# Performance work log

Measured on AMD Instinct MI355X. Metric: run time of the kernel, lower is better.

The kernel has to match this reference:

```python
import jax, jax.numpy as jnp
import numpy as np

B, D, H, W = 2, 256, 64, 64
NH = 4
EPS = 1e-5


def _ln(x, g, b):
    # LayerNorm over channel dim of NCHW tensor (matches permute->LN(C)->permute)
    mu = jnp.mean(x, axis=1, keepdims=True)
    var = jnp.mean((x - mu) ** 2, axis=1, keepdims=True)
    xn = (x - mu) * jax.lax.rsqrt(var + EPS)
    return xn * g[None, :, None, None] + b[None, :, None, None]


def _conv1x1(x, w, b):
    # w: (out_c, in_c)
    return jnp.einsum('bchw,oc->bohw', x, w) + b[None, :, None, None]


def _dwconv3x3(x, w, b):
    # depthwise 3x3, w: (C, 1, 3, 3)
    y = jax.lax.conv_general_dilated(
        x, w, window_strides=(1, 1), padding='SAME',
        dimension_numbers=('NCHW', 'OIHW', 'NCHW'), feature_group_count=D)
    return y + b[None, :, None, None]


def setup_inputs() -> dict:
    key = jax.random.key(0)
    ks = jax.random.split(key, 12)
    sc = 0.02

    def n(k, shape):
        return jax.random.normal(k, shape, dtype=jnp.float32) * sc

    return {
        'image_embedding': jax.random.normal(ks[0], (B, D, H, W), dtype=jnp.float32),
        'guide': jax.random.normal(ks[1], (B, D, H, W), dtype=jnp.float32),
        'ln1_g': jnp.ones((D,), jnp.float32), 'ln1_b': jnp.zeros((D,), jnp.float32),
        'ln2_g': jnp.ones((D,), jnp.float32), 'ln2_b': jnp.zeros((D,), jnp.float32),
        'qw1': n(ks[2], (D, D)), 'qb1': jnp.zeros((D,), jnp.float32),
        'qw2': n(ks[3], (D, 1, 3, 3)), 'qb2': jnp.zeros((D,), jnp.float32),
        'kw1': n(ks[4], (D, D)), 'kb1': jnp.zeros((D,), jnp.float32),
        'kw2': n(ks[5], (D, 1, 3, 3)), 'kb2': jnp.zeros((D,), jnp.float32),
        'vw1': n(ks[6], (D, D)), 'vb1': jnp.zeros((D,), jnp.float32),
        'vw2': n(ks[7], (D, 1, 3, 3)), 'vb2': jnp.zeros((D,), jnp.float32),
        'ow': n(ks[8], (D, D)), 'ob': jnp.zeros((D,), jnp.float32),
    }


def reference(image_embedding, guide, ln1_g, ln1_b, ln2_g, ln2_b,
              qw1, qb1, qw2, qb2, kw1, kb1, kw2, kb2,
              vw1, vb1, vw2, vb2, ow, ob):
    residual = image_embedding
    x = _ln(image_embedding, ln1_g, ln1_b)
    g = _ln(guide, ln2_g, ln2_b)

    q = _dwconv3x3(_conv1x1(x, qw1, qb1), qw2, qb2)
    k = _dwconv3x3(_conv1x1(g, kw1, kb1), kw2, kb2)
    v = _dwconv3x3(_conv1x1(g, vw1, vb1), vw2, vb2)

    hd = D // NH
    scale = hd ** -0.5

    def to_heads(t):  # (B,C,H,W) -> (B, NH, HW, hd)
        return t.reshape(B, NH, hd, H * W).transpose(0, 1, 3, 2)

    q = to_heads(q) * scale
    k = to_heads(k)
    v = to_heads(v)

    attn = jax.nn.softmax(jnp.einsum('bhnd,bhmd->bhnm', q, k), axis=-1)
    out = jnp.einsum('bhnm,bhmd->bhnd', attn, v)
    out = out.transpose(0, 1, 3, 2).reshape(B, D, H, W)
    out = _conv1x1(out, ow, ob)
    return residual + out
```

## Files before the change

kernel.cpp:

```cpp
#include <hip/hip_runtime.h>
#include <cstdint>
#include <cstddef>

typedef unsigned short u16;
typedef unsigned int u32;
typedef __attribute__((ext_vector_type(8))) short short8;
typedef __attribute__((ext_vector_type(4))) float f32x4;
typedef __attribute__((ext_vector_type(16))) float f32x16;
typedef __attribute__((ext_vector_type(2))) unsigned int u32x2;

#define CD 256
#define HWD 4096
#define NHD 4
#define HDD 64
#define NSPLIT 4

static __device__ __forceinline__ u16 f2b(float f) {
    u32 u = __builtin_bit_cast(u32, f);
    return (u16)((u + 0x7fffu + ((u >> 16) & 1u)) >> 16);
}
static __device__ __forceinline__ float b2f(u16 h) {
    return __builtin_bit_cast(float, (u32)h << 16);
}
static __device__ __forceinline__ u32 pk2(float a, float b) {
    return (u32)f2b(a) | ((u32)f2b(b) << 16);
}
static __device__ __forceinline__ float fexp2(float x) {
#if __has_builtin(__builtin_amdgcn_exp2f)
    return __builtin_amdgcn_exp2f(x);
#else
    return __expf(x * 0.69314718056f);
#endif
}
static __device__ __forceinline__ u32 cvtpk(float lo, float hi) {
    u32 r;
    asm("v_cvt_pk_bf16_f32 %0, %1, %2" : "=v"(r) : "v"(lo), "v"(hi));
    return r;
}
static __device__ __forceinline__ u32x2 plswap(u32 a, u32 b) {
    return __builtin_amdgcn_permlane32_swap(a, b, false, false);
}
static __device__ __forceinline__ void async16(const void* g, void* l) {
    __builtin_amdgcn_global_load_lds(
        (const __attribute__((address_space(1))) unsigned int*)g,
        (__attribute__((address_space(3))) unsigned int*)l,
        16, 0, 0);
}

__global__ __launch_bounds__(256) void ln_transpose(
    const float* __restrict__ x0, const float* __restrict__ x1,
    const float* __restrict__ g0, const float* __restrict__ b0,
    const float* __restrict__ g1, const float* __restrict__ b1,
    const float* __restrict__ qw1, const float* __restrict__ kw1,
    const float* __restrict__ vw1, const float* __restrict__ ow,
    u16* __restrict__ out0, u16* __restrict__ out1, u16* __restrict__ wbf)
{
    int bid = blockIdx.x;
    int tid = threadIdx.x;

    if (bid >= 512) {
        int base = (bid - 512) * 8192 + tid * 32;
        int which = base >> 16;
        int off = base & 65535;
        const float* s = (which == 0) ? qw1 : (which == 1) ? kw1
                       : (which == 2) ? vw1 : ow;
        s += off;
        u16* d = wbf + (size_t)which * 65536 + off;
        #pragma unroll
        for (int j = 0; j < 4; ++j) {
            float4 a = ((const float4*)s)[2 * j];
            float4 b = ((const float4*)s)[2 * j + 1];
            uint4 o;
            o.x = pk2(a.x, a.y); o.y = pk2(a.z, a.w);
            o.z = pk2(b.x, b.y); o.w = pk2(b.z, b.w);
            ((uint4*)d)[j] = o;
        }
        return;
    }

    int t = bid >> 8, b = (bid >> 7) & 1, p0 = (bid & 127) << 5;
    const float* x = t ? x1 : x0;
    const float* g = t ? g1 : g0;
    const float* bb = t ? b1 : b0;
    u16* out = t ? out1 : out0;

    int tx = tid & 31, ty = tid >> 5;
    const float* xb = x + (size_t)b * CD * HWD + p0 + tx;

    __shared__ float red[2][8][32];
    __shared__ u16 T[256][33];

    float xv[32];
    float s = 0.f, sq = 0.f;
    #pragma unroll
    for (int i = 0; i < 32; ++i) {
        float v = xb[(size_t)(ty * 32 + i) * HWD];
        xv[i] = v;
        s += v; sq += v * v;
    }
    red[0][ty][tx] = s; red[1][ty][tx] = sq;
    __syncthreads();
    float st = 0.f, sqt = 0.f;
    #pragma unroll
    for (int j = 0; j < 8; ++j) { st += red[0][j][tx]; sqt += red[1][j][tx]; }
    float mean = st * (1.f / 256.f);
    float var = sqt * (1.f / 256.f) - mean * mean;
    float rstd = rsqrtf(var + 1e-5f);

    #pragma unroll
    for (int i = 0; i < 32; ++i) {
        int c = ty * 32 + i;
        float v = (xv[i] - mean) * rstd * g[c] + bb[c];
        T[c][tx] = f2b(v);
    }
    __syncthreads();

    #pragma unroll
    for (int pass = 0; pass < 4; ++pass) {
        int idx = pass * 256 + tid;
        int p = idx >> 5, cs = (idx & 31) * 8;
        u16 tmp[8];
        #pragma unroll
        for (int j = 0; j < 8; ++j) tmp[j] = T[cs + j][p];
        *(uint4*)&out[((size_t)b * HWD + p0 + p) * CD + cs] = *(const uint4*)tmp;
    }
}

__global__ __launch_bounds__(256) void qkv_gemm(
    const u16* __restrict__ xT, const u16* __restrict__ gT,
    const u16* __restrict__ Wbf,
    const float* __restrict__ qb1, const float* __restrict__ kb1,
    const float* __restrict__ vb1,
    u16* __restrict__ q1, u16* __restrict__ k1, u16* __restrict__ v1)
{
    int z = blockIdx.z;
    int mm = z >> 1, b = z & 1;
    const u16* X    = (mm == 0) ? xT : gT;
    const u16* W    = Wbf + (size_t)mm * 65536;
    const float* Bi = (mm == 0) ? qb1 : (mm == 1) ? kb1 : vb1;
    u16* Y          = (mm == 0) ? q1 : (mm == 1) ? k1 : v1;

    int n0 = blockIdx.x * 128;
    int p0 = blockIdx.y * 64;

    __shared__ u16 As[64][72];
    __shared__ u16 Bs[128][72];

    int tid = threadIdx.x;
    int lane = tid & 63, w = tid >> 6;
    int wm = w >> 1, wn = w & 1;
    int l15 = lane & 15, quad = lane >> 4;

    f32x4 acc[2][4];
    #pragma unroll
    for (int mi = 0; mi < 2; ++mi)
        #pragma unroll
        for (int nj = 0; nj < 4; ++nj)
            acc[mi][nj] = (f32x4){0.f, 0.f, 0.f, 0.f};

    const u16* Xb = X + (size_t)b * HWD * CD;

    int arow = tid >> 2, aseg = (tid & 3) * 16;
    const u16* agp = Xb + (size_t)(p0 + arow) * CD + aseg;
    int brow = tid >> 1, bkh = (tid & 1) * 32;
    const u16* wgp = W + (size_t)(n0 + brow) * CD + bkh;

    uint4 ra0 = ((const uint4*)agp)[0], ra1 = ((const uint4*)agp)[1];
    uint4 rb0 = ((const uint4*)wgp)[0], rb1 = ((const uint4*)wgp)[1];
    uint4 rb2 = ((const uint4*)wgp)[2], rb3 = ((const uint4*)wgp)[3];

    for (int kt = 0; kt < 4; ++kt) {
        __syncthreads();
        *(uint4*)&As[arow][aseg] = ra0;
        *(uint4*)&As[arow][aseg + 8] = ra1;
        *(uint4*)&Bs[brow][bkh] = rb0;
        *(uint4*)&Bs[brow][bkh + 8] = rb1;
        *(uint4*)&Bs[brow][bkh + 16] = rb2;
        *(uint4*)&Bs[brow][bkh + 24] = rb3;
        if (kt < 3) {
            const u16* ag2 = agp + (kt + 1) * 64;
            ra0 = ((const uint4*)ag2)[0]; ra1 = ((const uint4*)ag2)[1];
            const u16* wg2 = wgp + (kt + 1) * 64;
            rb0 = ((const uint4*)wg2)[0]; rb1 = ((const uint4*)wg2)[1];
            rb2 = ((const uint4*)wg2)[2]; rb3 = ((const uint4*)wg2)[3];
        }
        __syncthreads();

        #pragma unroll
        for (int kk = 0; kk < 2; ++kk) {
            short8 af[2], bf[4];
            #pragma unroll
            for (int mi = 0; mi < 2; ++mi)
                af[mi] = *(const short8*)&As[wm * 32 + mi * 16 + l15][kk * 32 + quad * 8];
            #pragma unroll
            for (int nj = 0; nj < 4; ++nj)
                bf[nj] = *(const short8*)&Bs[wn * 64 + nj * 16 + l15][kk * 32 + quad * 8];
            #pragma unroll
            for (int mi = 0; mi < 2; ++mi)
                #pragma unroll
                for (int nj = 0; nj < 4; ++nj)
                    acc[mi][nj] = __builtin_amdgcn_mfma_f32_16x16x32_bf16(
                        af[mi], bf[nj], acc[mi][nj], 0, 0, 0);
        }
    }

    u16* Yb = Y + (size_t)b * HWD * CD;
    float bias[4];
    #pragma unroll
    for (int nj = 0; nj < 4; ++nj)
        bias[nj] = Bi[n0 + wn * 64 + nj * 16 + l15];
    #pragma unroll
    for (int mi = 0; mi < 2; ++mi) {
        #pragma unroll
        for (int r = 0; r < 4; ++r) {
            int p = p0 + wm * 32 + mi * 16 + quad * 4 + r;
            #pragma unroll
            for (int nj = 0; nj < 4; ++nj) {
                int ch = n0 + wn * 64 + nj * 16 + l15;
                Yb[(size_t)p * CD + ch] = f2b(acc[mi][nj][r] + bias[nj]);
            }
        }
    }
}

#define LOADROW(r, hh)                                                      \
    if ((hh) < 0 || (hh) >= 64) {                                           \
        _Pragma("unroll") for (int j = 0; j < 18; ++j) r[j] = 0.f;          \
    } else {                                                                \
        const u16* rp = inb + (size_t)((hh) * 64) * CD;                     \
        r[0] = (w0 > 0) ? b2f(rp[(size_t)(w0 - 1) * CD]) : 0.f;             \
        _Pragma("unroll") for (int j = 1; j <= 16; ++j)                     \
            r[j] = b2f(rp[(size_t)(w0 - 1 + j) * CD]);                      \
        r[17] = (w0 < 48) ? b2f(rp[(size_t)(w0 + 16) * CD]) : 0.f;          \
    }

#define CONVROW(hh, ra, rb, rc)                                             \
    {                                                                       \
        float accv[16];                                                     \
        _Pragma("unroll") for (int pi = 0; pi < 16; ++pi)                   \
            accv[pi] = bias                                                 \
              + w9[0] * ra[pi] + w9[1] * ra[pi + 1] + w9[2] * ra[pi + 2]    \
              + w9[3] * rb[pi] + w9[4] * rb[pi + 1] + w9[5] * rb[pi + 2]    \
              + w9[6] * rc[pi] + w9[7] * rc[pi + 1] + w9[8] * rc[pi + 2];   \
        int p0 = (hh) * 64 + w0;                                            \
        if (which == 2) {                                                   \
            u32 w8[8];                                                      \
            _Pragma("unroll") for (int j = 0; j < 8; ++j)                   \
                w8[j] = pk2(accv[2 * j], accv[2 * j + 1]);                  \
            uint4* dst = (uint4*)(Vt + ((size_t)(b * CD + c)) * HWD + p0);  \
            dst[0] = make_uint4(w8[0], w8[1], w8[2], w8[3]);                \
            dst[1] = make_uint4(w8[4], w8[5], w8[6], w8[7]);                \
        } else {                                                            \
            u16* outp = ((which == 0) ? Q : K) + (size_t)b * HWD * CD;      \
            _Pragma("unroll") for (int pi = 0; pi < 16; ++pi)               \
                outp[(size_t)(p0 + pi) * CD + c] = f2b(accv[pi] * oscale);  \
        }                                                                   \
    }

__global__ __launch_bounds__(256) void dwconv_nc(
    const u16* __restrict__ q1, const u16* __restrict__ k1, const u16* __restrict__ v1,
    const float* __restrict__ qw2, const float* __restrict__ qb2,
    const float* __restrict__ kw2, const float* __restrict__ kb2,
    const float* __restrict__ vw2, const float* __restrict__ vb2,
    u16* __restrict__ Q, u16* __restrict__ K, u16* __restrict__ Vt)
{
    int bid = blockIdx.x;
    int which = bid >> 8;
    int rem = bid & 255;
    int b = rem >> 7;
    int hp = (rem >> 2) & 31;
    int ws = rem & 3;
    int h0 = hp * 2, w0 = ws * 16;

    const u16* in = ((which == 0) ? q1 : (which == 1) ? k1 : v1) + (size_t)b * HWD * CD;
    const float* wsrc = (which == 0) ? qw2 : (which == 1) ? kw2 : vw2;
    const float* bsrc = (which == 0) ? qb2 : (which == 1) ? kb2 : vb2;
    float oscale = (which == 0) ? 0.18033688011112042f : 1.0f;

    int c = threadIdx.x;
    float w9[9];
    #pragma unroll
    for (int j = 0; j < 9; ++j) w9[j] = wsrc[c * 9 + j];
    float bias = bsrc[c];

    const u16* inb = in + c;

    float r0[18], r1[18], r2[18];
    LOADROW(r0, h0 - 1)
    LOADROW(r1, h0)
    LOADROW(r2, h0 + 1)
    CONVROW(h0, r0, r1, r2)
    LOADROW(r0, h0 + 2)
    CONVROW(h0 + 1, r1, r2, r0)
}

__global__ __launch_bounds__(256, 4) void attn_kernel(
    const u16* __restrict__ Q, const u16* __restrict__ K,
    const u16* __restrict__ Vt, u16* __restrict__ Opart,
    float* __restrict__ Psum)
{
    int qt = blockIdx.x;
    int bh = blockIdx.y;
    int ks = blockIdx.z;
    int b = bh >> 2, nh = bh & 3;

    __shared__ u16 Ks_[2][64 * 64];
    __shared__ u16 Vs_[2][64 * 64];

    int tid = threadIdx.x;
    int lane = tid & 63, w = tid >> 6;
    int l31 = lane & 31, h = lane >> 5;
    int sw = l31 & 7;

    const u16* Qb = Q + ((size_t)b * HWD) * CD + nh * 64;
    const u16* Kb = K + ((size_t)b * HWD) * CD + nh * 64;
    const u16* Vb = Vt + ((size_t)bh * HDD) * HWD;

    int q0 = qt * 128 + w * 32;

    short8 qf[4];
    #pragma unroll
    for (int si = 0; si < 4; ++si)
        qf[si] = *(const short8*)(Qb + (size_t)(q0 + l31) * CD + si * 16 + h * 8);

    int rr = lane >> 3;
    int gseg = (lane & 7) ^ rr;
    const u16* kgb = Kb + (size_t)(ks * 1024 + w * 16 + rr) * CD + gseg * 8;
    const u16* vgb = Vb + (size_t)(w * 16 + rr) * HWD + ks * 1024 + gseg * 8;

    f32x16 acc[2];
    #pragma unroll
    for (int db = 0; db < 2; ++db)
        #pragma unroll
        for (int r = 0; r < 16; ++r) acc[db][r] = 0.f;
    float psum = 0.f;

    #pragma unroll
    for (int j = 0; j < 2; ++j) {
        async16(kgb + (size_t)(j * 8) * CD, &Ks_[0][(w * 16 + j * 8) * 64]);
        async16(vgb + (size_t)(j * 8) * HWD, &Vs_[0][(w * 16 + j * 8) * 64]);
    }

    for (int it = 0; it < 16; ++it) {
        int cur = it & 1;
        __syncthreads();
        if (it + 1 < 16) {
            int nxt = cur ^ 1;
            #pragma unroll
            for (int j = 0; j < 2; ++j) {
                async16(kgb + (size_t)((it + 1) * 64 + j * 8) * CD,
                        &Ks_[nxt][(w * 16 + j * 8) * 64]);
                async16(vgb + (size_t)(j * 8) * HWD + (it + 1) * 64,
                        &Vs_[nxt][(w * 16 + j * 8) * 64]);
            }
        }

        #pragma unroll
        for (int kb = 0; kb < 2; ++kb) {
            short8 kf[4];
            #pragma unroll
            for (int si = 0; si < 4; ++si)
                kf[si] = *(const short8*)&Ks_[cur][(kb * 32 + l31) * 64 +
                                                   (((si * 2 + h) ^ sw) << 3)];
            f32x16 st;
            #pragma unroll
            for (int r = 0; r < 16; ++r) st[r] = 0.f;
            __builtin_amdgcn_s_setprio(1);
            #pragma unroll
            for (int si = 0; si < 4; ++si)
                st = __builtin_amdgcn_mfma_f32_32x32x16_bf16(
                    kf[si], qf[si], st, 0, 0, 0);
            __builtin_amdgcn_s_setprio(0);

            float e[16];
            #pragma unroll
            for (int r = 0; r < 16; ++r) e[r] = fexp2(st[r]);
            #pragma unroll
            for (int r = 0; r < 16; r += 4)
                psum += (e[r] + e[r + 1]) + (e[r + 2] + e[r + 3]);

            u32 wv[8];
            #pragma unroll
            for (int m = 0; m < 8; ++m) wv[m] = cvtpk(e[2 * m], e[2 * m + 1]);
            u32x2 s02 = plswap(wv[0], wv[2]);
            u32x2 s13 = plswap(wv[1], wv[3]);
            u32x2 s46 = plswap(wv[4], wv[6]);
            u32x2 s57 = plswap(wv[5], wv[7]);
            union { u32 u[4]; short8 s8; } p0_, p1_;
            p0_.u[0] = s02.x; p0_.u[1] = s13.x; p0_.u[2] = s02.y; p0_.u[3] = s13.y;
            p1_.u[0] = s46.x; p1_.u[1] = s57.x; p1_.u[2] = s46.y; p1_.u[3] = s57.y;

            #pragma unroll
            for (int db = 0; db < 2; ++db) {
                short8 vf0 = *(const short8*)&Vs_[cur][(db * 32 + l31) * 64 +
                                 ((((kb * 2 + 0) * 2 + h) ^ sw) << 3)];
                short8 vf1 = *(const short8*)&Vs_[cur][(db * 32 + l31) * 64 +
                                 ((((kb * 2 + 1) * 2 + h) ^ sw) << 3)];
                __builtin_amdgcn_s_setprio(1);
                acc[db] = __builtin_amdgcn_mfma_f32_32x32x16_bf16(
                    p0_.s8, vf0, acc[db], 0, 0, 0);
                acc[db] = __builtin_amdgcn_mfma_f32_32x32x16_bf16(
                    p1_.s8, vf1, acc[db], 0, 0, 0);
                __builtin_amdgcn_s_setprio(0);
            }
        }
    }

    u16* Ob = Opart + (((size_t)ks * 8 + bh) * HWD) * HDD;
    #pragma unroll
    for (int db = 0; db < 2; ++db)
        #pragma unroll
        for (int r = 0; r < 16; ++r) {
            int n = q0 + (r & 3) + 8 * (r >> 2) + 4 * h;
            Ob[(size_t)n * HDD + db * 32 + l31] = f2b(acc[db][r]);
        }

    float s = psum + __shfl_xor(psum, 32);
    float* Pb = Psum + ((size_t)ks * 8 + bh) * HWD + q0;
    if (lane < 32) Pb[lane] = s;
}

__global__ __launch_bounds__(256) void out_gemm(
    const u16* __restrict__ Wo, const float* __restrict__ Bi,
    const u16* __restrict__ Opart, const float* __restrict__ Psum,
    const float* __restrict__ residual, float* __restrict__ out)
{
    int b = blockIdx.z;
    int m0 = blockIdx.y * 64;
    int n0 = blockIdx.x * 64;

    __shared__ u16 As[64][40];
    __shared__ u16 Bs[64][40];

    int tid = threadIdx.x;
    int lane = tid & 63, w = tid >> 6;
    int wm = w >> 1, wn = w & 1;
    int l15 = lane & 15, quad = lane >> 4;

    f32x4 acc[2][2];
    #pragma unroll
    for (int mi = 0; mi < 2; ++mi)
        #pragma unroll
        for (int nj = 0; nj < 2; ++nj)
            acc[mi][nj] = (f32x4){0.f, 0.f, 0.f, 0.f};

    int arow = tid >> 2, aseg = (tid & 3) * 8;
    const u16* wgp = Wo + (size_t)(m0 + arow) * CD + aseg;
    int brow = tid >> 2, bseg = (tid & 3) * 8;
    int pn = n0 + brow;

    uint4 ra = *(const uint4*)wgp;

    uint4 ro[NSPLIT]; float rinv;
    {
        int c = bseg;
        int bh = b * 4 + (c >> 6), d0 = c & 63;
        float p = 0.f;
        #pragma unroll
        for (int s = 0; s < NSPLIT; ++s) {
            ro[s] = *(const uint4*)&Opart[(((size_t)s * 8 + bh) * HWD + pn) * HDD + d0];
            p += Psum[((size_t)s * 8 + bh) * HWD + pn];
        }
        rinv = 1.f / p;
    }

    for (int kt = 0; kt < 8; ++kt) {
        __syncthreads();
        *(uint4*)&As[arow][aseg] = ra;
        {
            float v[8];
            #pragma unroll
            for (int j = 0; j < 8; ++j) v[j] = 0.f;
            #pragma unroll
            for (int s = 0; s < NSPLIT; ++s) {
                u16 t[8];
                *(uint4*)t = ro[s];
                #pragma unroll
                for (int j = 0; j < 8; ++j) v[j] += b2f(t[j]);
            }
            uint4 bb;
            bb.x = pk2(v[0] * rinv, v[1] * rinv);
            bb.y = pk2(v[2] * rinv, v[3] * rinv);
            bb.z = pk2(v[4] * rinv, v[5] * rinv);
            bb.w = pk2(v[6] * rinv, v[7] * rinv);
            *(uint4*)&Bs[brow][bseg] = bb;
        }
        if (kt < 7) {
            ra = *(const uint4*)(wgp + (kt + 1) * 32);
            int c = (kt + 1) * 32 + bseg;
            int bh = b * 4 + (c >> 6), d0 = c & 63;
            float p = 0.f;
            #pragma unroll
            for (int s = 0; s < NSPLIT; ++s) {
                ro[s] = *(const uint4*)&Opart[(((size_t)s * 8 + bh) * HWD + pn) * HDD + d0];
                p += Psum[((size_t)s * 8 + bh) * HWD + pn];
            }
            rinv = 1.f / p;
        }
        __syncthreads();

        short8 af[2], bf[2];
        #pragma unroll
        for (int mi = 0; mi < 2; ++mi)
            af[mi] = *(const short8*)&As[wm * 32 + mi * 16 + l15][quad * 8];
        #pragma unroll
        for (int nj = 0; nj < 2; ++nj)
            bf[nj] = *(const short8*)&Bs[wn * 32 + nj * 16 + l15][quad * 8];
        #pragma unroll
        for (int mi = 0; mi < 2; ++mi)
            #pragma unroll
            for (int nj = 0; nj < 2; ++nj)
                acc[mi][nj] = __builtin_amdgcn_mfma_f32_16x16x32_bf16(
                    af[mi], bf[nj], acc[mi][nj], 0, 0, 0);
    }

    #pragma unroll
    for (int mi = 0; mi < 2; ++mi) {
        int mb = m0 + wm * 32 + mi * 16 + quad * 4;
        #pragma unroll
        for (int r = 0; r < 4; ++r) {
            float bias = Bi[mb + r];
            const float* res = residual + (size_t)(b * CD + mb + r) * HWD;
            float* o = out + (size_t)(b * CD + mb + r) * HWD;
            #pragma unroll
            for (int nj = 0; nj < 2; ++nj) {
                int n = n0 + wn * 32 + nj * 16 + l15;
                o[n] = acc[mi][nj][r] + bias + res[n];
            }
        }
    }
}

extern "C" void kernel_launch(void* const* d_in, const int* in_sizes, int n_in,
                              void* d_out, int out_size, void* d_ws, size_t ws_size,
                              hipStream_t stream) {
    (void)in_sizes; (void)n_in; (void)out_size; (void)ws_size;

    const float* image = (const float*)d_in[0];
    const float* guide = (const float*)d_in[1];
    const float* ln1_g = (const float*)d_in[2];
    const float* ln1_b = (const float*)d_in[3];
    const float* ln2_g = (const float*)d_in[4];
    const float* ln2_b = (const float*)d_in[5];
    const float* qw1 = (const float*)d_in[6];
    const float* qb1 = (const float*)d_in[7];
    const float* qw2 = (const float*)d_in[8];
    const float* qb2 = (const float*)d_in[9];
    const float* kw1 = (const float*)d_in[10];
    const float* kb1 = (const float*)d_in[11];
    const float* kw2 = (const float*)d_in[12];
    const float* kb2 = (const float*)d_in[13];
    const float* vw1 = (const float*)d_in[14];
    const float* vb1 = (const float*)d_in[15];
    const float* vw2 = (const float*)d_in[16];
    const float* vb2 = (const float*)d_in[17];
    const float* ow  = (const float*)d_in[18];
    const float* ob  = (const float*)d_in[19];
    float* out = (float*)d_out;

    char* ws = (char*)d_ws;
    u16* xT    = (u16*)(ws + (size_t)0  * (1 << 20));
    u16* gT    = (u16*)(ws + (size_t)4  * (1 << 20));
    u16* q1    = (u16*)(ws + (size_t)8  * (1 << 20));
    u16* k1    = (u16*)(ws + (size_t)12 * (1 << 20));
    u16* v1    = (u16*)(ws + (size_t)16 * (1 << 20));
    u16* Qh    = (u16*)(ws + (size_t)20 * (1 << 20));
    u16* Kh    = (u16*)(ws + (size_t)24 * (1 << 20));
    u16* Vt    = (u16*)(ws + (size_t)28 * (1 << 20));
    u16*   Opart = (u16*)(ws + (size_t)0  * (1 << 20));
    float* Psum  = (float*)(ws + (size_t)18 * (1 << 20));
    u16*   Wbf   = (u16*)(ws + (size_t)33 * (1 << 20));

    ln_transpose<<<dim3(544), dim3(256), 0, stream>>>(
        image, guide, ln1_g, ln1_b, ln2_g, ln2_b,
        qw1, kw1, vw1, ow, xT, gT, Wbf);

    qkv_gemm<<<dim3(2, 64, 6), dim3(256), 0, stream>>>(
        xT, gT, Wbf, qb1, kb1, vb1, q1, k1, v1);

    dwconv_nc<<<dim3(768), dim3(256), 0, stream>>>(
        q1, k1, v1, qw2, qb2, kw2, kb2, vw2, vb2, Qh, Kh, Vt);

    attn_kernel<<<dim3(32, 8, NSPLIT), dim3(256), 0, stream>>>(Qh, Kh, Vt, Opart, Psum);

    out_gemm<<<dim3(64, 4, 2), dim3(256), 0, stream>>>(
        Wbf + (size_t)3 * 65536, ob, Opart, Psum, image, out);
}
```

Before: 176.0 us.

## Load full K=256 tiles into XOR-swizzled LDS in qkv and out GEMMs

Both the QKV projection GEMM and the output GEMM now load the whole 256-deep K dimension for a 64x64 tile into shared memory at once, using an XOR swizzle on 16-byte chunks to avoid bank conflicts. This removes the per-K-step sync loop. The QKV GEMM's N tile shrinks from 128 to 64, doubling the grid to get more blocks. The cost is 64 KB of LDS per block, which may limit occupancy, plus more global loads in flight per thread and more re-reads of the activations.

New measurement: 188.3 us. +7.0%, slower.

```diff
diff --git a/kernel.cpp b/kernel.cpp
--- a/kernel.cpp
+++ b/kernel.cpp
@@ -140,83 +140,75 @@
     const float* Bi = (mm == 0) ? qb1 : (mm == 1) ? kb1 : vb1;
     u16* Y          = (mm == 0) ? q1 : (mm == 1) ? k1 : v1;
 
-    int n0 = blockIdx.x * 128;
+    int n0 = blockIdx.x * 64;
     int p0 = blockIdx.y * 64;
 
-    __shared__ u16 As[64][72];
-    __shared__ u16 Bs[128][72];
+    __shared__ u16 As[64 * 256];
+    __shared__ u16 Bs[64 * 256];
 
     int tid = threadIdx.x;
     int lane = tid & 63, w = tid >> 6;
     int wm = w >> 1, wn = w & 1;
     int l15 = lane & 15, quad = lane >> 4;
-
-    f32x4 acc[2][4];
+    int sw = l15 & 7;
+
+    int row = tid >> 2, seg = tid & 3;
+    const u16* agp = X + ((size_t)b * HWD + p0 + row) * CD + seg * 64;
+    const u16* wgp = W + (size_t)(n0 + row) * CD + seg * 64;
+
+    uint4 ra[8], rb[8];
+    #pragma unroll
+    for (int j = 0; j < 8; ++j) ra[j] = ((const uint4*)agp)[j];
+    #pragma unroll
+    for (int j = 0; j < 8; ++j) rb[j] = ((const uint4*)wgp)[j];
+
+    #pragma unroll
+    for (int j = 0; j < 8; ++j) {
+        int ch = (seg * 8 + j) ^ (row & 7);
+        *(uint4*)&As[row * 256 + ch * 8] = ra[j];
+        *(uint4*)&Bs[row * 256 + ch * 8] = rb[j];
+    }
+    __syncthreads();
+
+    f32x4 acc[2][2];
     #pragma unroll
     for (int mi = 0; mi < 2; ++mi)
         #pragma unroll
-        for (int nj = 0; nj < 4; ++nj)
+        for (int nj = 0; nj < 2; ++nj)
             acc[mi][nj] = (f32x4){0.f, 0.f, 0.f, 0.f};
 
-    const u16* Xb = X + (size_t)b * HWD * CD;
-
-    int arow = tid >> 2, aseg = (tid & 3) * 16;
-    const u16* agp = Xb + (size_t)(p0 + arow) * CD + aseg;
-    int brow = tid >> 1, bkh = (tid & 1) * 32;
-    const u16* wgp = W + (size_t)(n0 + brow) * CD + bkh;
-
-    uint4 ra0 = ((const uint4*)agp)[0], ra1 = ((const uint4*)agp)[1];
-    uint4 rb0 = ((const uint4*)wgp)[0], rb1 = ((const uint4*)wgp)[1];
-    uint4 rb2 = ((const uint4*)wgp)[2], rb3 = ((const uint4*)wgp)[3];
-
-    for (int kt = 0; kt < 4; ++kt) {
-        __syncthreads();
-        *(uint4*)&As[arow][aseg] = ra0;
-        *(uint4*)&As[arow][aseg + 8] = ra1;
-        *(uint4*)&Bs[brow][bkh] = rb0;
-        *(uint4*)&Bs[brow][bkh + 8] = rb1;
-        *(uint4*)&Bs[brow][bkh + 16] = rb2;
-        *(uint4*)&Bs[brow][bkh + 24] = rb3;
-        if (kt < 3) {
-            const u16* ag2 = agp + (kt + 1) * 64;
-            ra0 = ((const uint4*)ag2)[0]; ra1 = ((const uint4*)ag2)[1];
-            const u16* wg2 = wgp + (kt + 1) * 64;
-            rb0 = ((const uint4*)wg2)[0]; rb1 = ((const uint4*)wg2)[1];
-            rb2 = ((const uint4*)wg2)[2]; rb3 = ((const uint4*)wg2)[3];
-        }
-        __syncthreads();
-
-        #pragma unroll
-        for (int kk = 0; kk < 2; ++kk) {
-            short8 af[2], bf[4];
-            #pragma unroll
-            for (int mi = 0; mi < 2; ++mi)
-                af[mi] = *(const short8*)&As[wm * 32 + mi * 16 + l15][kk * 32 + quad * 8];
-            #pragma unroll
-            for (int nj = 0; nj < 4; ++nj)
-                bf[nj] = *(const short8*)&Bs[wn * 64 + nj * 16 + l15][kk * 32 + quad * 8];
-            #pragma unroll
-            for (int mi = 0; mi < 2; ++mi)
-                #pragma unroll
-                for (int nj = 0; nj < 4; ++nj)
-                    acc[mi][nj] = __builtin_amdgcn_mfma_f32_16x16x32_bf16(
-                        af[mi], bf[nj], acc[mi][nj], 0, 0, 0);
-        }
+    #pragma unroll
+    for (int ks = 0; ks < 8; ++ks) {
+        short8 af[2], bf[2];
+        #pragma unroll
+        for (int mi = 0; mi < 2; ++mi)
+            af[mi] = *(const short8*)&As[(wm * 32 + mi * 16 + l15) * 256 +
+                                         (((ks * 4 + quad) ^ sw) << 3)];
+        #pragma unroll
+        for (int nj = 0; nj < 2; ++nj)
+            bf[nj] = *(const short8*)&Bs[(wn * 32 + nj * 16 + l15) * 256 +
+                                         (((ks * 4 + quad) ^ sw) << 3)];
+        #pragma unroll
+        for (int mi = 0; mi < 2; ++mi)
+            #pragma unroll
+            for (int nj = 0; nj < 2; ++nj)
+                acc[mi][nj] = __builtin_amdgcn_mfma_f32_16x16x32_bf16(
+                    af[mi], bf[nj], acc[mi][nj], 0, 0, 0);
     }
 
     u16* Yb = Y + (size_t)b * HWD * CD;
-    float bias[4];
-    #pragma unroll
-    for (int nj = 0; nj < 4; ++nj)
-        bias[nj] = Bi[n0 + wn * 64 + nj * 16 + l15];
+    float bias[2];
+    #pragma unroll
+    for (int nj = 0; nj < 2; ++nj)
+        bias[nj] = Bi[n0 + wn * 32 + nj * 16 + l15];
     #pragma unroll
     for (int mi = 0; mi < 2; ++mi) {
         #pragma unroll
         for (int r = 0; r < 4; ++r) {
             int p = p0 + wm * 32 + mi * 16 + quad * 4 + r;
             #pragma unroll
-            for (int nj = 0; nj < 4; ++nj) {
-                int ch = n0 + wn * 64 + nj * 16 + l15;
+            for (int nj = 0; nj < 2; ++nj) {
+                int ch = n0 + wn * 32 + nj * 16 + l15;
                 Yb[(size_t)p * CD + ch] = f2b(acc[mi][nj][r] + bias[nj]);
             }
         }
@@ -429,13 +421,60 @@
     int m0 = blockIdx.y * 64;
     int n0 = blockIdx.x * 64;
 
-    __shared__ u16 As[64][40];
-    __shared__ u16 Bs[64][40];
+    __shared__ u16 As[64 * 256];
+    __shared__ u16 Bs[64 * 256];
 
     int tid = threadIdx.x;
     int lane = tid & 63, w = tid >> 6;
     int wm = w >> 1, wn = w & 1;
     int l15 = lane & 15, quad = lane >> 4;
+    int sw = l15 & 7;
+
+    int row = tid >> 2, seg = tid & 3;
+
+    const u16* wgp = Wo + (size_t)(m0 + row) * CD + seg * 64;
+    uint4 ra[8];
+    #pragma unroll
+    for (int j = 0; j < 8; ++j) ra[j] = ((const uint4*)wgp)[j];
+
+    int pn = n0 + row;
+    int bh = b * 4 + seg;
+    float p = 0.f;
+    #pragma unroll
+    for (int s = 0; s < NSPLIT; ++s)
+        p += Psum[((size_t)s * 8 + bh) * HWD + pn];
+    float rinv = 1.f / p;
+
+    uint4 rb[8];
+    #pragma unroll
+    for (int j = 0; j < 8; ++j) {
+        float v[8];
+        #pragma unroll
+        for (int k = 0; k < 8; ++k) v[k] = 0.f;
+        #pragma unroll
+        for (int s = 0; s < NSPLIT; ++s) {
+            uint4 t4 = *(const uint4*)&Opart[
+                (((size_t)s * 8 + bh) * HWD + pn) * HDD + j * 8];
+            u16 tt[8];
+            *(uint4*)tt = t4;
+            #pragma unroll
+            for (int k = 0; k < 8; ++k) v[k] += b2f(tt[k]);
+        }
+        uint4 o;
+        o.x = pk2(v[0] * rinv, v[1] * rinv);
+        o.y = pk2(v[2] * rinv, v[3] * rinv);
+        o.z = pk2(v[4] * rinv, v[5] * rinv);
+        o.w = pk2(v[6] * rinv, v[7] * rinv);
+        rb[j] = o;
+    }
+
+    #pragma unroll
+    for (int j = 0; j < 8; ++j) {
+        int ch = (seg * 8 + j) ^ (row & 7);
+        *(uint4*)&As[row * 256 + ch * 8] = ra[j];
+        *(uint4*)&Bs[row * 256 + ch * 8] = rb[j];
+    }
+    __syncthreads();
 
     f32x4 acc[2][2];
     #pragma unroll
@@ -444,68 +483,17 @@
         for (int nj = 0; nj < 2; ++nj)
             acc[mi][nj] = (f32x4){0.f, 0.f, 0.f, 0.f};
 
-    int arow = tid >> 2, aseg = (tid & 3) * 8;
-    const u16* wgp = Wo + (size_t)(m0 + arow) * CD + aseg;
-    int brow = tid >> 2, bseg = (tid & 3) * 8;
-    int pn = n0 + brow;
-
-    uint4 ra = *(const uint4*)wgp;
-
-    uint4 ro[NSPLIT]; float rinv;
-    {
-        int c = bseg;
-        int bh = b * 4 + (c >> 6), d0 = c & 63;
-        float p = 0.f;
-        #pragma unroll
-        for (int s = 0; s < NSPLIT; ++s) {
-            ro[s] = *(const uint4*)&Opart[(((size_t)s * 8 + bh) * HWD + pn) * HDD + d0];
-            p += Psum[((size_t)s * 8 + bh) * HWD + pn];
-        }
-        rinv = 1.f / p;
-    }
-
-    for (int kt = 0; kt < 8; ++kt) {
-        __syncthreads();
-        *(uint4*)&As[arow][aseg] = ra;
-        {
-            float v[8];
-            #pragma unroll
-            for (int j = 0; j < 8; ++j) v[j] = 0.f;
-            #pragma unroll
-            for (int s = 0; s < NSPLIT; ++s) {
-                u16 t[8];
-                *(uint4*)t = ro[s];
-                #pragma unroll
-                for (int j = 0; j < 8; ++j) v[j] += b2f(t[j]);
-            }
-            uint4 bb;
-            bb.x = pk2(v[0] * rinv, v[1] * rinv);
-            bb.y = pk2(v[2] * rinv, v[3] * rinv);
-            bb.z = pk2(v[4] * rinv, v[5] * rinv);
-            bb.w = pk2(v[6] * rinv, v[7] * rinv);
-            *(uint4*)&Bs[brow][bseg] = bb;
-        }
-        if (kt < 7) {
-            ra = *(const uint4*)(wgp + (kt + 1) * 32);
-            int c = (kt + 1) * 32 + bseg;
-            int bh = b * 4 + (c >> 6), d0 = c & 63;
-            float p = 0.f;
-            #pragma unroll
-            for (int s = 0; s < NSPLIT; ++s) {
-                ro[s] = *(const uint4*)&Opart[(((size_t)s * 8 + bh) * HWD + pn) * HDD + d0];
-                p += Psum[((size_t)s * 8 + bh) * HWD + pn];
-            }
-            rinv = 1.f / p;
-        }
-        __syncthreads();
-
+    #pragma unroll
+    for (int ks = 0; ks < 8; ++ks) {
         short8 af[2], bf[2];
         #pragma unroll
         for (int mi = 0; mi < 2; ++mi)
-            af[mi] = *(const short8*)&As[wm * 32 + mi * 16 + l15][quad * 8];
+            af[mi] = *(const short8*)&As[(wm * 32 + mi * 16 + l15) * 256 +
+                                         (((ks * 4 + quad) ^ sw) << 3)];
         #pragma unroll
         for (int nj = 0; nj < 2; ++nj)
-            bf[nj] = *(const short8*)&Bs[wn * 32 + nj * 16 + l15][quad * 8];
+            bf[nj] = *(const short8*)&Bs[(wn * 32 + nj * 16 + l15) * 256 +
+                                         (((ks * 4 + quad) ^ sw) << 3)];
         #pragma unroll
         for (int mi = 0; mi < 2; ++mi)
             #pragma unroll
@@ -575,7 +563,7 @@
         image, guide, ln1_g, ln1_b, ln2_g, ln2_b,
         qw1, kw1, vw1, ow, xT, gT, Wbf);
 
-    qkv_gemm<<<dim3(2, 64, 6), dim3(256), 0, stream>>>(
+    qkv_gemm<<<dim3(4, 64, 6), dim3(256), 0, stream>>>(
         xT, gT, Wbf, qb1, kb1, vb1, q1, k1, v1);
 
     dwconv_nc<<<dim3(768), dim3(256), 0, stream>>>(
```
